# Optimization experiments

Hardware: AMD Instinct MI355X
Metric: run time of the kernel (lower is better)

The kernel has to match this reference:

```python
import jax, jax.numpy as jnp
import numpy as np

NEG_RATIO = 5          # neg_sample_ratio, also k (num_nodes-1 >> ratio)
THRESH = 0.7           # hard_neg_threshold
SMOOTH = 0.1           # label_smoothing
NUM_NODES = 200_000
DIM = 128
B = 1024               # batch size, all labels == 1 (all positives)
FILL_VAL = -1.0e9


def _l2_normalize(x, eps=1e-12):
    # F.normalize(p=2, dim=-1): divide by clamped L2 norm
    n = jnp.sqrt(jnp.sum(x * x, axis=-1, keepdims=True))
    return x / jnp.maximum(n, eps)


def setup_inputs() -> dict:
    key = jax.random.key(0)
    k1, k2, k3, k4 = jax.random.split(key, 4)
    src_nodes = jax.random.randint(k1, (B,), 0, NUM_NODES)
    dst_nodes = jax.random.randint(k2, (B,), 0, NUM_NODES)
    labels = jnp.ones((B,), dtype=jnp.float32)  # all positives -> pos_mask all True
    timestamps = jax.random.uniform(k3, (B,), dtype=jnp.float32)
    memory = jax.random.normal(k4, (NUM_NODES, DIM), dtype=jnp.float32)
    return {
        "src_nodes": src_nodes,
        "dst_nodes": dst_nodes,
        "labels": labels,
        "timestamps": timestamps,
        "memory": memory,
    }


def reference(src_nodes, dst_nodes, labels, timestamps, memory):
    # --- embedding gather + L2 normalize ---
    src_emb = memory[src_nodes]                      # [B, D]
    s = _l2_normalize(src_emb).astype(jnp.float16)   # use_half_precision=True
    c = _l2_normalize(memory).astype(jnp.float16)    # [N, D]

    # --- similarity [B, N], back to fp32 ---
    sim = jnp.matmul(s, c.T).astype(jnp.float32)

    # --- mask out ground-truth dst and below-threshold sims ---
    cols = jnp.arange(NUM_NODES)
    allowed = cols[None, :] != dst_nodes[:, None]    # exclude GT positives
    valid = allowed & (sim > THRESH)
    score = jnp.where(valid, sim, FILL_VAL)

    # --- top-k hard negatives per positive ---
    k = NEG_RATIO  # min(neg_sample_ratio, num_nodes-1)
    topk_vals, topk_idx = jax.lax.top_k(score, k)    # [B, k]
    is_real = (topk_vals > FILL_VAL + 1.0).reshape(-1)  # [B*k]

    # --- fallback random negatives (fixed-shape equivalent of the torch
    #     pack-real-then-pad-random assembly; total count == B*k either way) ---
    rkey = jax.random.key(42)
    rand_dst = jax.random.randint(rkey, (B * k,), 0, NUM_NODES)
    src_rep = jnp.repeat(src_nodes, k)               # [B*k]
    rand_dst = jnp.where(rand_dst == src_rep, (rand_dst + 1) % NUM_NODES, rand_dst)

    final_src = src_rep
    final_dst = jnp.where(is_real, topk_idx.reshape(-1), rand_dst)
    neg_ts = jnp.repeat(timestamps, k)

    # --- assemble augmented batch ---
    new_src = jnp.concatenate([src_nodes, final_src])
    new_dst = jnp.concatenate([dst_nodes, final_dst])
    new_labels = jnp.concatenate([labels, jnp.zeros((B * k,), labels.dtype)])
    new_ts = jnp.concatenate([timestamps, neg_ts])

    # --- label smoothing ---
    new_labels = new_labels * (1.0 - SMOOTH) + (1.0 - new_labels) * SMOOTH

    return new_src, new_dst, new_labels, new_ts, topk_vals
```

## Files before the change

kernel.cpp:

```cpp
#include <hip/hip_runtime.h>

#define NUM_NODES 200000
#define DIM 128
#define BATCH 1024
#define K_NEG 5
#define CAP 16
#define NBLK 250
#define CPB 800
#define TCOL 32
#define THRESH 0.7f
#define FILL (-1.0e9f)

typedef __attribute__((ext_vector_type(8))) short short8;
typedef __attribute__((ext_vector_type(16))) float f32x16;

__device__ __forceinline__ unsigned short f2bf(float x) {
  unsigned u = __builtin_bit_cast(unsigned, x);
  return (unsigned short)((u + 0x7fffu + ((u >> 16) & 1u)) >> 16);
}

__device__ __forceinline__ void stage16(const void* g, void* l) {
  __builtin_amdgcn_global_load_lds(
      (const __attribute__((address_space(1))) unsigned int*)g,
      (__attribute__((address_space(3))) unsigned int*)l,
      16, 0, 0);
}

__device__ __forceinline__ void tf2x32(unsigned k0, unsigned k1,
                                       unsigned x0, unsigned x1,
                                       unsigned* o0, unsigned* o1) {
  unsigned ks2 = k0 ^ k1 ^ 0x1BD11BDAu;
  unsigned v0 = x0 + k0, v1 = x1 + k1;
#define TFR(r) { v0 += v1; v1 = (v1 << r) | (v1 >> (32 - r)); v1 ^= v0; }
  TFR(13) TFR(15) TFR(26) TFR(6)   v0 += k1;  v1 += ks2 + 1u;
  TFR(17) TFR(29) TFR(16) TFR(24)  v0 += ks2; v1 += k0 + 2u;
  TFR(13) TFR(15) TFR(26) TFR(6)   v0 += k0;  v1 += k1 + 3u;
  TFR(17) TFR(29) TFR(16) TFR(24)  v0 += k1;  v1 += ks2 + 4u;
  TFR(13) TFR(15) TFR(26) TFR(6)   v0 += ks2; v1 += k0 + 5u;
#undef TFR
  *o0 = v0; *o1 = v1;
}

__device__ __forceinline__ unsigned rbits32(unsigned ka, unsigned kb, unsigned m) {
  unsigned o0, o1;
  tf2x32(ka, kb, 0u, m, &o0, &o1);
  return o0 ^ o1;
}

__global__ void prep_kernel(const float* __restrict__ memory,
                            const int* __restrict__ src_nodes,
                            unsigned short* __restrict__ s16f,
                            int* __restrict__ cand_cnt) {
  int tid = threadIdx.x;
  int gid = blockIdx.x * 256 + tid;
  if (gid < BATCH) cand_cnt[gid] = 0;
  int row = blockIdx.x * 4 + (tid >> 6);
  int L = tid & 63;
  int s = src_nodes[row];
  float2 v = ((const float2*)(memory + (size_t)s * DIM))[L];
  float ss = v.x * v.x + v.y * v.y;
#pragma unroll
  for (int off = 32; off > 0; off >>= 1) ss += __shfl_xor(ss, off);
  float inv = 1.0f / fmaxf(sqrtf(ss), 1e-12f);
  unsigned p = (unsigned)f2bf(v.x * inv) | ((unsigned)f2bf(v.y * inv) << 16);
  int ms = row >> 5, l32 = row & 31;
  int c = L >> 2;
  int ks = c >> 1, half = c & 1;
  ((unsigned*)s16f)[(((ms * 8 + ks) * 64) + half * 32 + l32) * 4 + (L & 3)] = p;
}

__global__ __launch_bounds__(512, 2) void sim_scan_kernel(
    const float* __restrict__ memory,
    const unsigned short* __restrict__ s16f,
    const int* __restrict__ dst_nodes,
    int* __restrict__ cand_cnt,
    float* __restrict__ cand_val,
    int* __restrict__ cand_idx) {
  __shared__ char bbuf[2][16384];

  int tid = threadIdx.x;
  int wid = tid >> 6;
  int lane = tid & 63;
  int half = lane >> 5;
  int l32 = lane & 31;
  int jb0 = blockIdx.x * CPB;

  {
    const char* mb = (const char*)memory;
    int i1 = tid;
    stage16(mb + (size_t)(jb0 + (i1 & 31)) * 512 + ((i1 >> 5) << 4),
            (char*)&bbuf[0][0] + (wid << 10));
    int i2 = tid + 512;
    stage16(mb + (size_t)(jb0 + (i2 & 31)) * 512 + ((i2 >> 5) << 4),
            (char*)&bbuf[0][0] + 8192 + (wid << 10));
  }

  const short8* __restrict__ af = (const short8*)s16f;
  short8 a[4][8];
#pragma unroll
  for (int m = 0; m < 4; ++m)
#pragma unroll
    for (int ks = 0; ks < 8; ++ks)
      a[m][ks] = af[(((wid * 4 + m) * 8) + ks) * 64 + lane];

  f32x16 Z;
#pragma unroll
  for (int i = 0; i < 16; ++i) Z[i] = 0.0f;

  __syncthreads();
  int cur = 0;

  for (int t = 0; t < 25; ++t) {
    if (t < 24) {
      const char* mb = (const char*)memory;
      int jn = jb0 + (t + 1) * TCOL;
      int i1 = tid;
      stage16(mb + (size_t)(jn + (i1 & 31)) * 512 + ((i1 >> 5) << 4),
              (char*)&bbuf[cur ^ 1][0] + (wid << 10));
      int i2 = tid + 512;
      stage16(mb + (size_t)(jn + (i2 & 31)) * 512 + ((i2 >> 5) << 4),
              (char*)&bbuf[cur ^ 1][0] + 8192 + (wid << 10));
    }

    const float4* lbp = (const float4*)(&bbuf[cur][0] + (half << 10) + (l32 << 4));
    short8 bf[8];
    float ss = 0.0f;
#pragma unroll
    for (int ks = 0; ks < 8; ++ks) {
      float4 q0 = lbp[ks * 128];
      float4 q1 = lbp[ks * 128 + 32];
      ss += q0.x * q0.x + q0.y * q0.y + q0.z * q0.z + q0.w * q0.w;
      ss += q1.x * q1.x + q1.y * q1.y + q1.z * q1.z + q1.w * q1.w;
      short8 f;
      f[0] = (short)f2bf(q0.x); f[1] = (short)f2bf(q0.y);
      f[2] = (short)f2bf(q0.z); f[3] = (short)f2bf(q0.w);
      f[4] = (short)f2bf(q1.x); f[5] = (short)f2bf(q1.y);
      f[6] = (short)f2bf(q1.z); f[7] = (short)f2bf(q1.w);
      bf[ks] = f;
    }
    ss += __shfl_xor(ss, 32);
    float nrm = fmaxf(sqrtf(ss), 1e-12f);
    float inv = 1.0f / nrm;
    float thr = THRESH * nrm;
    int gj = jb0 + t * TCOL + l32;

#pragma unroll
    for (int mp = 0; mp < 2; ++mp) {
      f32x16 accA = __builtin_amdgcn_mfma_f32_32x32x16_bf16(a[mp * 2][0], bf[0], Z, 0, 0, 0);
      f32x16 accB = __builtin_amdgcn_mfma_f32_32x32x16_bf16(a[mp * 2 + 1][0], bf[0], Z, 0, 0, 0);
#pragma unroll
      for (int ks = 1; ks < 8; ++ks) {
        accA = __builtin_amdgcn_mfma_f32_32x32x16_bf16(a[mp * 2][ks], bf[ks], accA, 0, 0, 0);
        accB = __builtin_amdgcn_mfma_f32_32x32x16_bf16(a[mp * 2 + 1][ks], bf[ks], accB, 0, 0, 0);
      }
      float mA = accA[0], mB = accB[0];
#pragma unroll
      for (int i = 1; i < 16; ++i) { mA = fmaxf(mA, accA[i]); mB = fmaxf(mB, accB[i]); }
      if (mA > thr || mB > thr) {
#pragma unroll
        for (int e = 0; e < 2; ++e) {
          int ms = wid * 4 + mp * 2 + e;
#pragma unroll
          for (int r = 0; r < 16; ++r) {
            float raw = (e == 0) ? accA[r] : accB[r];
            if (raw > thr) {
              int gi = ms * 32 + (r & 3) + 8 * (r >> 2) + 4 * half;
              if (gj != dst_nodes[gi]) {
                int p = atomicAdd(&cand_cnt[gi], 1);
                if (p < CAP) {
                  cand_val[gi * CAP + p] = raw * inv;
                  cand_idx[gi * CAP + p] = gj;
                }
              }
            }
          }
        }
      }
    }

    __syncthreads();
    cur ^= 1;
  }
}

__global__ void finalize_kernel(const int* __restrict__ src_nodes,
                                const int* __restrict__ dst_nodes,
                                const float* __restrict__ labels,
                                const float* __restrict__ ts,
                                const int* __restrict__ cand_cnt,
                                const float* __restrict__ cand_val,
                                const int* __restrict__ cand_idx,
                                float* __restrict__ out) {
  int r = blockIdx.x * 256 + threadIdx.x;
  if (r >= BATCH) return;
  const int TOT = BATCH + BATCH * K_NEG;
  int srcv = src_nodes[r];
  float tsv = ts[r];
  out[r] = (float)srcv;
  out[TOT + r] = (float)dst_nodes[r];
  float l = labels[r];
  out[2 * TOT + r] = l * 0.9f + (1.0f - l) * 0.1f;
  out[3 * TOT + r] = tsv;

  int cnt = cand_cnt[r];
  cnt = cnt < CAP ? cnt : CAP;
  float cv[CAP]; int ci[CAP];
  for (int i = 0; i < cnt; ++i) { cv[i] = cand_val[r * CAP + i]; ci[i] = cand_idx[r * CAP + i]; }

  unsigned k1a, k1b, k2a, k2b;
  tf2x32(0u, 42u, 0u, 0u, &k1a, &k1b);
  tf2x32(0u, 42u, 0u, 1u, &k2a, &k2b);

  const unsigned span = 200000u;
  const unsigned mult = 167296u;

  for (int s = 0; s < K_NEG; ++s) {
    int sel = -1;
    for (int i = 0; i < cnt; ++i)
      if (sel < 0 || cv[i] > cv[sel] || (cv[i] == cv[sel] && ci[i] < ci[sel])) sel = i;
    float v = FILL; int idx = 0;
    if (sel >= 0) { v = cv[sel]; idx = ci[sel]; cv[sel] = FILL; ci[sel] = 0x7fffffff; }
    bool is_real = v > (FILL + 1.0f);

    unsigned m = (unsigned)(r * K_NEG + s);
    unsigned hi = rbits32(k1a, k1b, m);
    unsigned lo = rbits32(k2a, k2b, m);
    unsigned off = ((hi % span) * mult + (lo % span)) % span;
    int rd = (int)off;
    if (rd == srcv) rd = (rd + 1) % NUM_NODES;
    int fd = is_real ? idx : rd;

    int mi = (int)m;
    out[BATCH + mi] = (float)srcv;
    out[TOT + BATCH + mi] = (float)fd;
    out[2 * TOT + BATCH + mi] = 0.1f;
    out[3 * TOT + BATCH + mi] = tsv;
    out[4 * TOT + mi] = v;
  }
}

extern "C" void kernel_launch(void* const* d_in, const int* in_sizes, int n_in,
                              void* d_out, int out_size, void* d_ws, size_t ws_size,
                              hipStream_t stream) {
  const int* src = (const int*)d_in[0];
  const int* dst = (const int*)d_in[1];
  const float* labels = (const float*)d_in[2];
  const float* ts = (const float*)d_in[3];
  const float* memory = (const float*)d_in[4];
  float* out = (float*)d_out;

  char* ws = (char*)d_ws;
  unsigned short* s16f = (unsigned short*)ws;
  int* cand_cnt = (int*)(ws + 262144);
  float* cand_val = (float*)(ws + 266240);
  int* cand_idx = (int*)(ws + 331776);

  prep_kernel<<<256, 256, 0, stream>>>(memory, src, s16f, cand_cnt);
  sim_scan_kernel<<<NBLK, 512, 0, stream>>>(memory, s16f, dst, cand_cnt, cand_val, cand_idx);
  finalize_kernel<<<(BATCH + 255) / 256, 256, 0, stream>>>(src, dst, labels, ts,
                                                           cand_cnt, cand_val, cand_idx, out);
}
```

Baseline: 222.3 us.

## Convert B tiles to bf16 once per block into shared fragments, pipelined

```diff
diff --git a/kernel.cpp b/kernel.cpp
--- a/kernel.cpp
+++ b/kernel.cpp
@@ -8,6 +8,7 @@
 #define NBLK 250
 #define CPB 800
 #define TCOL 32
+#define NT 25
 #define THRESH 0.7f
 #define FILL (-1.0e9f)
 
@@ -76,7 +77,9 @@
     int* __restrict__ cand_cnt,
     float* __restrict__ cand_val,
     int* __restrict__ cand_idx) {
-  __shared__ char bbuf[2][16384];
+  __shared__ char rawb[16384];
+  __shared__ unsigned short fragb[2][4096];
+  __shared__ float nrmb[2][32];
 
   int tid = threadIdx.x;
   int wid = tid >> 6;
@@ -85,16 +88,35 @@
   int l32 = lane & 31;
   int jb0 = blockIdx.x * CPB;
 
-  {
-    const char* mb = (const char*)memory;
-    int i1 = tid;
-    stage16(mb + (size_t)(jb0 + (i1 & 31)) * 512 + ((i1 >> 5) << 4),
-            (char*)&bbuf[0][0] + (wid << 10));
-    int i2 = tid + 512;
-    stage16(mb + (size_t)(jb0 + (i2 & 31)) * 512 + ((i2 >> 5) << 4),
-            (char*)&bbuf[0][0] + 8192 + (wid << 10));
-  }
-
+  const char* mb = (const char*)memory;
+
+#define STAGE(t) {                                                              \
+    int jn = jb0 + (t) * TCOL;                                                  \
+    stage16(mb + (size_t)(jn + (tid & 31)) * 512 + ((tid >> 5) << 4),           \
+            (char*)rawb + (wid << 10));                                         \
+    stage16(mb + (size_t)(jn + (tid & 31)) * 512 + (((tid >> 5) + 16) << 4),    \
+            (char*)rawb + 8192 + (wid << 10));                                  \
+  }
+
+  int ccol = wid * 4 + (lane & 3);
+  int cseg = lane >> 2;
+#define CONVERT(p) {                                                            \
+    float4 q0 = *(const float4*)(rawb + (((2 * cseg) * 32 + ccol) << 4));       \
+    float4 q1 = *(const float4*)(rawb + (((2 * cseg + 1) * 32 + ccol) << 4));   \
+    float ss = q0.x * q0.x + q0.y * q0.y + q0.z * q0.z + q0.w * q0.w            \
+             + q1.x * q1.x + q1.y * q1.y + q1.z * q1.z + q1.w * q1.w;           \
+    ss += __shfl_xor(ss, 4); ss += __shfl_xor(ss, 8);                           \
+    ss += __shfl_xor(ss, 16); ss += __shfl_xor(ss, 32);                         \
+    short8 f;                                                                   \
+    f[0] = (short)f2bf(q0.x); f[1] = (short)f2bf(q0.y);                         \
+    f[2] = (short)f2bf(q0.z); f[3] = (short)f2bf(q0.w);                         \
+    f[4] = (short)f2bf(q1.x); f[5] = (short)f2bf(q1.y);                         \
+    f[6] = (short)f2bf(q1.z); f[7] = (short)f2bf(q1.w);                         \
+    *(short8*)((char*)fragb[p] + ((cseg * 32 + ccol) << 4)) = f;                \
+    if (cseg == 0) nrmb[p][ccol] = fmaxf(sqrtf(ss), 1e-12f);                    \
+  }
+
+  STAGE(0);
   const short8* __restrict__ af = (const short8*)s16f;
   short8 a[4][8];
 #pragma unroll
@@ -102,47 +124,30 @@
 #pragma unroll
     for (int ks = 0; ks < 8; ++ks)
       a[m][ks] = af[(((wid * 4 + m) * 8) + ks) * 64 + lane];
+  __syncthreads();
+  CONVERT(0);
+  __syncthreads();
+  STAGE(1);
+  __syncthreads();
 
   f32x16 Z;
 #pragma unroll
   for (int i = 0; i < 16; ++i) Z[i] = 0.0f;
 
-  __syncthreads();
-  int cur = 0;
-
-  for (int t = 0; t < 25; ++t) {
-    if (t < 24) {
-      const char* mb = (const char*)memory;
-      int jn = jb0 + (t + 1) * TCOL;
-      int i1 = tid;
-      stage16(mb + (size_t)(jn + (i1 & 31)) * 512 + ((i1 >> 5) << 4),
-              (char*)&bbuf[cur ^ 1][0] + (wid << 10));
-      int i2 = tid + 512;
-      stage16(mb + (size_t)(jn + (i2 & 31)) * 512 + ((i2 >> 5) << 4),
-              (char*)&bbuf[cur ^ 1][0] + 8192 + (wid << 10));
-    }
-
-    const float4* lbp = (const float4*)(&bbuf[cur][0] + (half << 10) + (l32 << 4));
+  for (int t = 0; t < NT; ++t) {
+    if (t < NT - 1) CONVERT((t + 1) & 1);
+    __syncthreads();
+    if (t < NT - 2) STAGE(t + 2);
+
+    int p = t & 1;
+    float nv = nrmb[p][l32];
+    float thr = THRESH * nv;
+    float invv = 1.0f / nv;
+    int gj = jb0 + t * TCOL + l32;
     short8 bf[8];
-    float ss = 0.0f;
-#pragma unroll
-    for (int ks = 0; ks < 8; ++ks) {
-      float4 q0 = lbp[ks * 128];
-      float4 q1 = lbp[ks * 128 + 32];
-      ss += q0.x * q0.x + q0.y * q0.y + q0.z * q0.z + q0.w * q0.w;
-      ss += q1.x * q1.x + q1.y * q1.y + q1.z * q1.z + q1.w * q1.w;
-      short8 f;
-      f[0] = (short)f2bf(q0.x); f[1] = (short)f2bf(q0.y);
-      f[2] = (short)f2bf(q0.z); f[3] = (short)f2bf(q0.w);
-      f[4] = (short)f2bf(q1.x); f[5] = (short)f2bf(q1.y);
-      f[6] = (short)f2bf(q1.z); f[7] = (short)f2bf(q1.w);
-      bf[ks] = f;
-    }
-    ss += __shfl_xor(ss, 32);
-    float nrm = fmaxf(sqrtf(ss), 1e-12f);
-    float inv = 1.0f / nrm;
-    float thr = THRESH * nrm;
-    int gj = jb0 + t * TCOL + l32;
+#pragma unroll
+    for (int ks = 0; ks < 8; ++ks)
+      bf[ks] = *(const short8*)((char*)fragb[p] + (((2 * ks + half) * 32 + l32) << 4));
 
 #pragma unroll
     for (int mp = 0; mp < 2; ++mp) {
@@ -159,17 +164,16 @@
       if (mA > thr || mB > thr) {
 #pragma unroll
         for (int e = 0; e < 2; ++e) {
-          int ms = wid * 4 + mp * 2 + e;
 #pragma unroll
           for (int r = 0; r < 16; ++r) {
             float raw = (e == 0) ? accA[r] : accB[r];
             if (raw > thr) {
-              int gi = ms * 32 + (r & 3) + 8 * (r >> 2) + 4 * half;
+              int gi = (wid * 4 + mp * 2 + e) * 32 + (r & 3) + 8 * (r >> 2) + 4 * half;
               if (gj != dst_nodes[gi]) {
-                int p = atomicAdd(&cand_cnt[gi], 1);
-                if (p < CAP) {
-                  cand_val[gi * CAP + p] = raw * inv;
-                  cand_idx[gi * CAP + p] = gj;
+                int pq = atomicAdd(&cand_cnt[gi], 1);
+                if (pq < CAP) {
+                  cand_val[gi * CAP + pq] = raw * invv;
+                  cand_idx[gi * CAP + pq] = gj;
                 }
               }
             }
@@ -179,8 +183,9 @@
     }
 
     __syncthreads();
-    cur ^= 1;
-  }
+  }
+#undef STAGE
+#undef CONVERT
 }
 
 __global__ void finalize_kernel(const int* __restrict__ src_nodes,
```

Result: faster. 188.5 us (-15.2%).
